# Performance work log

Measured on AMD Instinct MI355X. Metric: run time of the kernel, lower is better.

The kernel has to match this reference:

```python
import jax, jax.numpy as jnp
import numpy as np

NUM_CLASSES = 32
SIGMA = 0.02
LOG_SIGMA = float(np.log(SIGMA))
HALF_LOG_2PI = float(0.5 * np.log(2.0 * np.pi))


def _gcn(x, adj, W1, b1, W2, b2):
    # Two-layer GCN: h = relu(A x W1 + b1); out = A h W2 + b2
    h = jax.nn.relu(jnp.einsum('bij,bjf->bif', adj, x) @ W1 + b1)
    return jnp.einsum('bij,bjf->bif', adj, h) @ W2 + b2


def setup_inputs() -> dict:
    key = jax.random.key(0)
    ks = jax.random.split(key, 10)
    B, N, F = 64, 1024, 512
    x = jax.random.normal(ks[0], (B, N, F), dtype=jnp.float32)
    adj = jax.random.uniform(ks[1], (B, N, N), dtype=jnp.float32) / N  # row-scaled dense adjacency
    masks = jax.random.randint(ks[2], (B, N, F), 0, 2, dtype=jnp.int32)
    noise = jax.random.normal(ks[3], (B, N, F), dtype=jnp.float32)
    s = 0.05
    We1 = jax.random.normal(ks[4], (F, 30), dtype=jnp.float32) * s
    be1 = jnp.zeros((30,), dtype=jnp.float32)
    We2 = jax.random.normal(ks[5], (30, 18), dtype=jnp.float32) * s
    be2 = jnp.zeros((18,), dtype=jnp.float32)
    Wd1 = jax.random.normal(ks[6], (18, 30), dtype=jnp.float32) * s
    bd1 = jnp.zeros((30,), dtype=jnp.float32)
    Wd2 = jax.random.normal(ks[7], (30, F), dtype=jnp.float32) * s
    bd2 = jnp.zeros((F,), dtype=jnp.float32)
    return dict(x=x, adj=adj, masks=masks, noise=noise, We1=We1, be1=be1,
                We2=We2, be2=be2, Wd1=Wd1, bd1=bd1, Wd2=Wd2, bd2=bd2)


def reference(x, adj, masks, noise, We1, be1, We2, be2, Wd1, bd1, Wd2, bd2):
    enc = _gcn(x, adj, We1, be1, We2, be2)            # [B,N,18]
    dec = _gcn(enc, adj, Wd1, bd1, Wd2, bd2)          # [B,N,F]
    dec_act = jnp.concatenate(
        (jax.nn.softmax(dec[..., :NUM_CLASSES], axis=-1),
         jax.nn.sigmoid(dec[..., NUM_CLASSES:])), axis=-1)
    m = masks.astype(dec_act.dtype)
    # Vectorized masked reparameterized Gaussian sample: s = mu + sigma*eps
    sampled = dec_act + m * (SIGMA * noise)
    # log N(s; mu, sigma) = -eps^2/2 - log(sigma) - 0.5*log(2pi), summed over masked entries
    lp_elem = -0.5 * noise * noise - LOG_SIGMA - HALF_LOG_2PI
    log_probs = jnp.sum(m * lp_elem, axis=(1, 2))      # [B]
    return dec, sampled, log_probs
```

## Files before the change

### kernel.cpp

```cpp
#include <hip/hip_runtime.h>

#define B_ 64
#define NN 1024
#define FF 512

typedef float  fx4 __attribute__((ext_vector_type(4)));
typedef float  fx2 __attribute__((ext_vector_type(2)));
typedef int    ix4 __attribute__((ext_vector_type(4)));
typedef unsigned int   ux4i __attribute__((ext_vector_type(4)));
typedef unsigned int   ux2i __attribute__((ext_vector_type(2)));
typedef unsigned short us4  __attribute__((ext_vector_type(4)));
typedef short  sx8 __attribute__((ext_vector_type(8)));

#define FP8_SCALE   16384.0f
#define INV_SCALE   6.103515625e-5f

static __device__ __forceinline__ unsigned short f2bf(float f){
    union { float f; unsigned u; } v; v.f = f;
    unsigned r = v.u + 0x7FFFu + ((v.u >> 16) & 1u);
    return (unsigned short)(r >> 16);
}
static __device__ __forceinline__ float bf2f(unsigned short h){
    union { unsigned u; float f; } v; v.u = ((unsigned)h) << 16;
    return v.f;
}
static __device__ __forceinline__ unsigned cvt_pk_bf16(float lo, float hi){
    unsigned r;
    asm("v_cvt_pk_bf16_f32 %0, %1, %2" : "=v"(r) : "v"(lo), "v"(hi));
    return r;
}
static __device__ __forceinline__ sx8 pack_bf16x8(fx4 v0, fx4 v1){
    union { unsigned u[4]; sx8 s; } r;
    r.u[0] = cvt_pk_bf16(v0[0], v0[1]);
    r.u[1] = cvt_pk_bf16(v0[2], v0[3]);
    r.u[2] = cvt_pk_bf16(v1[0], v1[1]);
    r.u[3] = cvt_pk_bf16(v1[2], v1[3]);
    return r.s;
}
template<typename T>
static __device__ __forceinline__ T ntload(const T* p){ return __builtin_nontemporal_load(p); }
static __device__ __forceinline__ void ntstore4(float* p, fx4 v){
    __builtin_nontemporal_store(v, (fx4*)p);
}

__global__ __launch_bounds__(512) void k_xw1(
    const float* __restrict__ x, const float* __restrict__ We1,
    unsigned short* __restrict__ u1T){
    __shared__ unsigned short wls[32*512];
    int tid = threadIdx.x;
    for (int i = tid; i < 32*512; i += 512){
        int col = i >> 9, k = i & 511;
        float v = (col < 30) ? We1[k*30 + col] : 0.f;
        wls[col*512 + ((((k >> 3) ^ (col & 7)) << 3) | (k & 7))] = f2bf(v);
    }
    __syncthreads();
    int w = tid >> 6, l = tid & 63;
    int lr = l & 15, kq = l >> 4;
    int b = blockIdx.y;
    int rowb = blockIdx.x*128 + w*16;
    const float* xp = x + ((size_t)b*NN + rowb + lr)*FF + kq*8;
    fx4 acc0 = {0,0,0,0}, acc1 = {0,0,0,0};
    int c0 = lr, c1 = 16 + lr;
    #pragma unroll 4
    for (int kk = 0; kk < FF; kk += 32){
        fx4 v0 = ntload((const fx4*)(xp + kk));
        fx4 v1 = ntload((const fx4*)(xp + kk + 4));
        sx8 a = pack_bf16x8(v0, v1);
        int chunk = (kk >> 3) + kq;
        sx8 b0 = *(const sx8*)(wls + c0*512 + ((chunk ^ (c0 & 7)) << 3));
        sx8 b1 = *(const sx8*)(wls + c1*512 + ((chunk ^ (c1 & 7)) << 3));
        acc0 = __builtin_amdgcn_mfma_f32_16x16x32_bf16(a, b0, acc0, 0, 0, 0);
        acc1 = __builtin_amdgcn_mfma_f32_16x16x32_bf16(a, b1, acc1, 0, 0, 0);
    }
    int row0 = rowb + kq*4;
    us4 o0 = { f2bf(acc0[0]), f2bf(acc0[1]), f2bf(acc0[2]), f2bf(acc0[3]) };
    us4 o1 = { f2bf(acc1[0]), f2bf(acc1[1]), f2bf(acc1[2]), f2bf(acc1[3]) };
    *(us4*)(u1T + ((size_t)b*32 + c0)*NN + row0) = o0;
    *(us4*)(u1T + ((size_t)b*32 + c1)*NN + row0) = o1;
}

__global__ __launch_bounds__(256) void k_cvt_h1u2(
    const float* __restrict__ adjf, unsigned char* __restrict__ adj8,
    const unsigned short* __restrict__ uT, const float* __restrict__ be1,
    const float* __restrict__ We2, unsigned short* __restrict__ u2T){
    __shared__ unsigned short uts[32*NN];
    __shared__ unsigned short hls[128][34];
    __shared__ float wels[540];
    int tid = threadIdx.x;
    int rt = blockIdx.x, b = blockIdx.y;
    for (int i = tid; i < 540; i += 256) wels[i] = We2[i];
    const ux4i* src = (const ux4i*)(uT + (size_t)b*32*NN);
    #pragma unroll
    for (int i = 0; i < 16; i++){
        int j = tid + i*256;
        int c = j >> 7;
        ux4i v = src[j];
        *(ux4i*)((char*)uts + ((j*16) ^ ((c & 7) << 4))) = v;
    }
    __syncthreads();
    int w = tid >> 6, l = tid & 63;
    int lr = l & 15, lk = (l >> 4) * 8;
    size_t aoff = (size_t)b*NN*NN + (size_t)(rt*128 + w*32 + lr)*NN + lk;
    int c0 = lr, c1 = 16 + lr;
    fx4 acc00 = {0,0,0,0}, acc01 = {0,0,0,0}, acc10 = {0,0,0,0}, acc11 = {0,0,0,0};
    #pragma unroll 4
    for (int kk = 0; kk < NN; kk += 32){
        fx4 v00 = ntload((const fx4*)(adjf + aoff + kk));
        fx4 v01 = ntload((const fx4*)(adjf + aoff + kk + 4));
        fx4 v10 = ntload((const fx4*)(adjf + aoff + 16*NN + kk));
        fx4 v11 = ntload((const fx4*)(adjf + aoff + 16*NN + kk + 4));
        sx8 a0 = pack_bf16x8(v00, v01);
        sx8 a1 = pack_bf16x8(v10, v11);
        {
            const float S = FP8_SCALE;
            int d0 = __builtin_amdgcn_cvt_pk_fp8_f32(v00[0]*S, v00[1]*S, 0, false);
            d0     = __builtin_amdgcn_cvt_pk_fp8_f32(v00[2]*S, v00[3]*S, d0, true);
            int d1 = __builtin_amdgcn_cvt_pk_fp8_f32(v01[0]*S, v01[1]*S, 0, false);
            d1     = __builtin_amdgcn_cvt_pk_fp8_f32(v01[2]*S, v01[3]*S, d1, true);
            ux2i s0 = { (unsigned)d0, (unsigned)d1 };
            *(ux2i*)(adj8 + aoff + kk) = s0;
            int d2 = __builtin_amdgcn_cvt_pk_fp8_f32(v10[0]*S, v10[1]*S, 0, false);
            d2     = __builtin_amdgcn_cvt_pk_fp8_f32(v10[2]*S, v10[3]*S, d2, true);
            int d3 = __builtin_amdgcn_cvt_pk_fp8_f32(v11[0]*S, v11[1]*S, 0, false);
            d3     = __builtin_amdgcn_cvt_pk_fp8_f32(v11[2]*S, v11[3]*S, d3, true);
            ux2i s1 = { (unsigned)d2, (unsigned)d3 };
            *(ux2i*)(adj8 + aoff + 16*NN + kk) = s1;
        }
        int kb = (kk + lk) * 2;
        sx8 b0 = *(const sx8*)((const char*)uts + ((c0*2048 + kb) ^ ((c0 & 7) << 4)));
        sx8 b1 = *(const sx8*)((const char*)uts + ((c1*2048 + kb) ^ ((c1 & 7) << 4)));
        acc00 = __builtin_amdgcn_mfma_f32_16x16x32_bf16(a0, b0, acc00, 0, 0, 0);
        acc01 = __builtin_amdgcn_mfma_f32_16x16x32_bf16(a0, b1, acc01, 0, 0, 0);
        acc10 = __builtin_amdgcn_mfma_f32_16x16x32_bf16(a1, b0, acc10, 0, 0, 0);
        acc11 = __builtin_amdgcn_mfma_f32_16x16x32_bf16(a1, b1, acc11, 0, 0, 0);
    }
    float bias0 = (c0 < 30) ? be1[c0] : 0.f;
    float bias1 = (c1 < 30) ? be1[c1] : 0.f;
    int lq = l >> 4;
    #pragma unroll
    for (int mt = 0; mt < 2; mt++){
        int rl0 = w*32 + mt*16 + lq*4;
        fx4 am0 = mt ? acc10 : acc00;
        fx4 am1 = mt ? acc11 : acc01;
        #pragma unroll
        for (int ct = 0; ct < 2; ct++){
            fx4 a = ct ? am1 : am0;
            float bb = ct ? bias1 : bias0;
            int col = ct ? c1 : c0;
            #pragma unroll
            for (int j = 0; j < 4; j++)
                hls[rl0 + j][col] = f2bf(fmaxf(a[j] + bb, 0.f));
        }
    }
    __syncthreads();
    int row = tid >> 1, half = tid & 1;
    float h[30];
    #pragma unroll
    for (int j = 0; j < 30; j++) h[j] = bf2f(hls[row][j]);
    float acc2[9] = {0,0,0,0,0,0,0,0,0};
    #pragma unroll
    for (int j = 0; j < 30; j++){
        #pragma unroll
        for (int c = 0; c < 9; c++) acc2[c] += h[j]*wels[j*18 + half*9 + c];
    }
    unsigned short* base = u2T + (size_t)b*32*NN + rt*128 + row;
    #pragma unroll
    for (int c = 0; c < 9; c++)
        base[(size_t)(half*9 + c)*NN] = f2bf(acc2[c]*INV_SCALE);
    #pragma unroll
    for (int i = 0; i < 7; i++)
        base[(size_t)(18 + half*7 + i)*NN] = 0;
}

template<int RM>
__global__ __launch_bounds__(256) void k_adjf8(
    const unsigned char* __restrict__ adj8,
    const unsigned short* __restrict__ uT,
    const float* __restrict__ bias, int biasN, float oscale,
    unsigned short* __restrict__ outT){
    __shared__ unsigned short uts[32*NN];
    int tid = threadIdx.x;
    int rt = blockIdx.x, b = blockIdx.y;
    const ux4i* src = (const ux4i*)(uT + (size_t)b*32*NN);
    #pragma unroll
    for (int i = 0; i < 16; i++){
        int j = tid + i*256;
        int c = j >> 7;
        ux4i v = src[j];
        *(ux4i*)((char*)uts + ((j*16) ^ ((c & 7) << 4))) = v;
    }
    __syncthreads();
    int w = tid >> 6, l = tid & 63;
    int lr = l & 15, lk = (l >> 4) * 8;
    size_t aoff = (size_t)b*NN*NN + (size_t)(rt*128 + w*32 + lr)*NN + lk;
    int c0 = lr, c1 = 16 + lr;
    fx4 acc00 = {0,0,0,0}, acc01 = {0,0,0,0}, acc10 = {0,0,0,0}, acc11 = {0,0,0,0};
    #pragma unroll 4
    for (int kk = 0; kk < NN; kk += 32){
        ux2i q0 = *(const ux2i*)(adj8 + aoff + kk);
        ux2i q1 = *(const ux2i*)(adj8 + aoff + 16*NN + kk);
        fx2 f0 = __builtin_amdgcn_cvt_pk_f32_fp8((int)q0[0], false);
        fx2 f1 = __builtin_amdgcn_cvt_pk_f32_fp8((int)q0[0], true);
        fx2 f2 = __builtin_amdgcn_cvt_pk_f32_fp8((int)q0[1], false);
        fx2 f3 = __builtin_amdgcn_cvt_pk_f32_fp8((int)q0[1], true);
        fx2 g0 = __builtin_amdgcn_cvt_pk_f32_fp8((int)q1[0], false);
        fx2 g1 = __builtin_amdgcn_cvt_pk_f32_fp8((int)q1[0], true);
        fx2 g2 = __builtin_amdgcn_cvt_pk_f32_fp8((int)q1[1], false);
        fx2 g3 = __builtin_amdgcn_cvt_pk_f32_fp8((int)q1[1], true);
        union { unsigned u[4]; sx8 s; } A0, A1;
        A0.u[0] = cvt_pk_bf16(f0[0], f0[1]);
        A0.u[1] = cvt_pk_bf16(f1[0], f1[1]);
        A0.u[2] = cvt_pk_bf16(f2[0], f2[1]);
        A0.u[3] = cvt_pk_bf16(f3[0], f3[1]);
        A1.u[0] = cvt_pk_bf16(g0[0], g0[1]);
        A1.u[1] = cvt_pk_bf16(g1[0], g1[1]);
        A1.u[2] = cvt_pk_bf16(g2[0], g2[1]);
        A1.u[3] = cvt_pk_bf16(g3[0], g3[1]);
        int kb = (kk + lk) * 2;
        sx8 b0 = *(const sx8*)((const char*)uts + ((c0*2048 + kb) ^ ((c0 & 7) << 4)));
        sx8 b1 = *(const sx8*)((const char*)uts + ((c1*2048 + kb) ^ ((c1 & 7) << 4)));
        acc00 = __builtin_amdgcn_mfma_f32_16x16x32_bf16(A0.s, b0, acc00, 0, 0, 0);
        acc01 = __builtin_amdgcn_mfma_f32_16x16x32_bf16(A0.s, b1, acc01, 0, 0, 0);
        acc10 = __builtin_amdgcn_mfma_f32_16x16x32_bf16(A1.s, b0, acc10, 0, 0, 0);
        acc11 = __builtin_amdgcn_mfma_f32_16x16x32_bf16(A1.s, b1, acc11, 0, 0, 0);
    }
    float bias0 = 0.f, bias1 = 0.f;
    if (bias){
        if (c0 < biasN) bias0 = bias[c0];
        if (c1 < biasN) bias1 = bias[c1];
    }
    int lq = l >> 4;
    #pragma unroll
    for (int mt = 0; mt < 2; mt++){
        int row0 = rt*128 + w*32 + mt*16 + lq*4;
        fx4 am0 = mt ? acc10 : acc00;
        fx4 am1 = mt ? acc11 : acc01;
        #pragma unroll
        for (int ct = 0; ct < 2; ct++){
            fx4 a = ct ? am1 : am0;
            float bb = ct ? bias1 : bias0;
            int col = ct ? c1 : c0;
            us4 o;
            #pragma unroll
            for (int j = 0; j < 4; j++){
                float v = (a[j] + bb) * oscale;
                o[j] = f2bf(v);
            }
            if (RM){
                #pragma unroll
                for (int j = 0; j < 4; j++)
                    outT[((size_t)b*NN + row0 + j)*32 + col] = o[j];
            } else {
                *(us4*)(outT + ((size_t)b*32 + col)*NN + row0) = o;
            }
        }
    }
}

__global__ __launch_bounds__(256) void k_v1h2(
    const unsigned char* __restrict__ adj8,
    const unsigned short* __restrict__ encT,
    const float* __restrict__ Wd1, const float* __restrict__ bd1,
    unsigned short* __restrict__ h2T){
    __shared__ unsigned short uts[32*NN];
    __shared__ unsigned short vls[128][34];
    __shared__ float wd[540];
    __shared__ float bdl[30];
    int tid = threadIdx.x;
    int rt = blockIdx.x, b = blockIdx.y;
    for (int i = tid; i < 540; i += 256) wd[i] = Wd1[i];
    if (tid < 30) bdl[tid] = bd1[tid];
    const ux4i* src = (const ux4i*)(encT + (size_t)b*32*NN);
    #pragma unroll
    for (int i = 0; i < 16; i++){
        int j = tid + i*256;
        int c = j >> 7;
        ux4i v = src[j];
        *(ux4i*)((char*)uts + ((j*16) ^ ((c & 7) << 4))) = v;
    }
    __syncthreads();
    int w = tid >> 6, l = tid & 63;
    int lr = l & 15, lk = (l >> 4) * 8;
    size_t aoff = (size_t)b*NN*NN + (size_t)(rt*128 + w*32 + lr)*NN + lk;
    int c0 = lr, c1 = 16 + lr;
    fx4 acc00 = {0,0,0,0}, acc01 = {0,0,0,0}, acc10 = {0,0,0,0}, acc11 = {0,0,0,0};
    #pragma unroll 4
    for (int kk = 0; kk < NN; kk += 32){
        ux2i q0 = *(const ux2i*)(adj8 + aoff + kk);
        ux2i q1 = *(const ux2i*)(adj8 + aoff + 16*NN + kk);
        fx2 f0 = __builtin_amdgcn_cvt_pk_f32_fp8((int)q0[0], false);
        fx2 f1 = __builtin_amdgcn_cvt_pk_f32_fp8((int)q0[0], true);
        fx2 f2 = __builtin_amdgcn_cvt_pk_f32_fp8((int)q0[1], false);
        fx2 f3 = __builtin_amdgcn_cvt_pk_f32_fp8((int)q0[1], true);
        fx2 g0 = __builtin_amdgcn_cvt_pk_f32_fp8((int)q1[0], false);
        fx2 g1 = __builtin_amdgcn_cvt_pk_f32_fp8((int)q1[0], true);
        fx2 g2 = __builtin_amdgcn_cvt_pk_f32_fp8((int)q1[1], false);
        fx2 g3 = __builtin_amdgcn_cvt_pk_f32_fp8((int)q1[1], true);
        union { unsigned u[4]; sx8 s; } A0, A1;
        A0.u[0] = cvt_pk_bf16(f0[0], f0[1]);
        A0.u[1] = cvt_pk_bf16(f1[0], f1[1]);
        A0.u[2] = cvt_pk_bf16(f2[0], f2[1]);
        A0.u[3] = cvt_pk_bf16(f3[0], f3[1]);
        A1.u[0] = cvt_pk_bf16(g0[0], g0[1]);
        A1.u[1] = cvt_pk_bf16(g1[0], g1[1]);
        A1.u[2] = cvt_pk_bf16(g2[0], g2[1]);
        A1.u[3] = cvt_pk_bf16(g3[0], g3[1]);
        int kb = (kk + lk) * 2;
        sx8 b0 = *(const sx8*)((const char*)uts + ((c0*2048 + kb) ^ ((c0 & 7) << 4)));
        sx8 b1 = *(const sx8*)((const char*)uts + ((c1*2048 + kb) ^ ((c1 & 7) << 4)));
        acc00 = __builtin_amdgcn_mfma_f32_16x16x32_bf16(A0.s, b0, acc00, 0, 0, 0);
        acc01 = __builtin_amdgcn_mfma_f32_16x16x32_bf16(A0.s, b1, acc01, 0, 0, 0);
        acc10 = __builtin_amdgcn_mfma_f32_16x16x32_bf16(A1.s, b0, acc10, 0, 0, 0);
        acc11 = __builtin_amdgcn_mfma_f32_16x16x32_bf16(A1.s, b1, acc11, 0, 0, 0);
    }
    int lq = l >> 4;
    #pragma unroll
    for (int mt = 0; mt < 2; mt++){
        int rl0 = w*32 + mt*16 + lq*4;
        fx4 am0 = mt ? acc10 : acc00;
        fx4 am1 = mt ? acc11 : acc01;
        #pragma unroll
        for (int ct = 0; ct < 2; ct++){
            fx4 a = ct ? am1 : am0;
            int col = ct ? c1 : c0;
            #pragma unroll
            for (int j = 0; j < 4; j++)
                vls[rl0 + j][col] = f2bf(a[j]);
        }
    }
    __syncthreads();
    int row = tid >> 1, half = tid & 1;
    float v[18];
    #pragma unroll
    for (int j = 0; j < 18; j++) v[j] = bf2f(vls[row][j]);
    float acc2[15];
    #pragma unroll
    for (int c = 0; c < 15; c++) acc2[c] = 0.f;
    #pragma unroll
    for (int j = 0; j < 18; j++){
        #pragma unroll
        for (int c = 0; c < 15; c++) acc2[c] += v[j]*wd[j*30 + half*15 + c];
    }
    unsigned short* base = h2T + (size_t)b*32*NN + rt*128 + row;
    #pragma unroll
    for (int c = 0; c < 15; c++){
        int cc = half*15 + c;
        base[(size_t)cc*NN] = f2bf(fmaxf(acc2[c] + bdl[cc], 0.f)*INV_SCALE);
    }
    base[(size_t)(30 + half)*NN] = 0;
}

__global__ __launch_bounds__(1024) void k_v2dec(
    const unsigned char* __restrict__ adj8,
    const unsigned short* __restrict__ h2T,
    const float* __restrict__ Wd2, const float* __restrict__ bd2,
    const int* __restrict__ masks, const float* __restrict__ noise,
    float* __restrict__ dec, float* __restrict__ sampled, float* __restrict__ part){
    __shared__ __align__(16) char smem[127488];
    __shared__ float red[16];
    unsigned short* uts = (unsigned short*)smem;
    unsigned short* wls = (unsigned short*)smem;
    unsigned short* v2ls = (unsigned short*)(smem + 107008);
    int tid = threadIdx.x;
    int rt = blockIdx.x, b = blockIdx.y;
    int w = tid >> 6, l = tid & 63;
    int lr = l & 15, kq = l >> 4, lk = kq*8;
    const ux4i* src = (const ux4i*)(h2T + (size_t)b*32*NN);
    #pragma unroll
    for (int i = 0; i < 4; i++){
        int j = tid + i*1024;
        int c = j >> 7;
        ux4i v = src[j];
        *(ux4i*)((char*)uts + ((j*16) ^ ((c & 7) << 4))) = v;
    }
    __syncthreads();
    size_t aoff = (size_t)b*NN*NN + (size_t)(rt*256 + w*16 + lr)*NN + lk;
    int c0 = lr, c1 = 16 + lr;
    fx4 acc00 = {0,0,0,0}, acc01 = {0,0,0,0};
    #pragma unroll 4
    for (int kk = 0; kk < NN; kk += 32){
        ux2i q0 = *(const ux2i*)(adj8 + aoff + kk);
        fx2 f0 = __builtin_amdgcn_cvt_pk_f32_fp8((int)q0[0], false);
        fx2 f1 = __builtin_amdgcn_cvt_pk_f32_fp8((int)q0[0], true);
        fx2 f2 = __builtin_amdgcn_cvt_pk_f32_fp8((int)q0[1], false);
        fx2 f3 = __builtin_amdgcn_cvt_pk_f32_fp8((int)q0[1], true);
        union { unsigned u[4]; sx8 s; } A0;
        A0.u[0] = cvt_pk_bf16(f0[0], f0[1]);
        A0.u[1] = cvt_pk_bf16(f1[0], f1[1]);
        A0.u[2] = cvt_pk_bf16(f2[0], f2[1]);
        A0.u[3] = cvt_pk_bf16(f3[0], f3[1]);
        int kb = (kk + lk) * 2;
        sx8 b0 = *(const sx8*)((const char*)uts + ((c0*2048 + kb) ^ ((c0 & 7) << 4)));
        sx8 b1 = *(const sx8*)((const char*)uts + ((c1*2048 + kb) ^ ((c1 & 7) << 4)));
        acc00 = __builtin_amdgcn_mfma_f32_16x16x32_bf16(A0.s, b0, acc00, 0, 0, 0);
        acc01 = __builtin_amdgcn_mfma_f32_16x16x32_bf16(A0.s, b1, acc01, 0, 0, 0);
    }
    {
        int rl0 = w*16 + kq*4;
        #pragma unroll
        for (int ct = 0; ct < 2; ct++){
            fx4 a = ct ? acc01 : acc00;
            int col = ct ? c1 : c0;
            #pragma unroll
            for (int j = 0; j < 4; j++)
                v2ls[(rl0 + j)*40 + col] = f2bf(a[j]);
        }
    }
    __syncthreads();
    for (int i = tid; i < 512*32; i += 1024){
        int col = i & 511, k = i >> 9;
        float v = (k < 30) ? Wd2[k*512 + col] : 0.f;
        wls[col*40 + k] = f2bf(v);
    }
    __syncthreads();
    const float LPC = 2.9930844722234733f;
    float lpacc = 0.f;
    int growbase = b*NN + rt*256;
    for (int it = 0; it < 16; it++){
        int rb = it*16;
        float (*dls)[516] = (float(*)[516])(smem + 40960 + (it & 1)*33024);
        size_t offA = (size_t)(growbase + rb + w)*FF + l*8;
        ix4 mA0 = ntload((const ix4*)(masks + offA));
        ix4 mA1 = ntload((const ix4*)(masks + offA + 4));
        fx4 zA0 = ntload((const fx4*)(noise + offA));
        fx4 zA1 = ntload((const fx4*)(noise + offA + 4));
        sx8 a = *(const sx8*)(v2ls + (rb + lr)*40 + kq*8);
        #pragma unroll
        for (int i = 0; i < 2; i++){
            int c = (w + 16*i)*16 + lr;
            sx8 bb = *(const sx8*)(wls + c*40 + kq*8);
            fx4 acc = {0,0,0,0};
            acc = __builtin_amdgcn_mfma_f32_16x16x32_bf16(a, bb, acc, 0, 0, 0);
            float bi = bd2[c];
            #pragma unroll
            for (int j = 0; j < 4; j++)
                dls[kq*4 + j][c] = acc[j] + bi;
        }
        __syncthreads();
        {
            fx4 d0 = *(const fx4*)&dls[w][l*8];
            fx4 d1 = *(const fx4*)&dls[w][l*8 + 4];
            float av[8];
            #pragma unroll
            for (int i = 0; i < 4; i++){
                av[i]   = 1.f/(1.f + __expf(-d0[i]));
                av[4+i] = 1.f/(1.f + __expf(-d1[i]));
            }
            if (l < 4){
                float mx = d0[0];
                #pragma unroll
                for (int i = 1; i < 4; i++) mx = fmaxf(mx, d0[i]);
                #pragma unroll
                for (int i = 0; i < 4; i++) mx = fmaxf(mx, d1[i]);
                mx = fmaxf(mx, __shfl_xor(mx, 1, 4));
                mx = fmaxf(mx, __shfl_xor(mx, 2, 4));
                float e[8], ss = 0.f;
                #pragma unroll
                for (int i = 0; i < 4; i++){ e[i] = __expf(d0[i] - mx); ss += e[i]; }
                #pragma unroll
                for (int i = 0; i < 4; i++){ e[4+i] = __expf(d1[i] - mx); ss += e[4+i]; }
                ss += __shfl_xor(ss, 1, 4);
                ss += __shfl_xor(ss, 2, 4);
                float inv = 1.f / ss;
                #pragma unroll
                for (int i = 0; i < 8; i++) av[i] = e[i]*inv;
            }
            ntstore4(dec + offA,     d0);
            ntstore4(dec + offA + 4, d1);
            fx4 sm0, sm1;
            #pragma unroll
            for (int i = 0; i < 4; i++){
                float mi0 = (float)mA0[i], zi0 = zA0[i];
                float mi1 = (float)mA1[i], zi1 = zA1[i];
                sm0[i] = av[i]   + mi0*(0.02f*zi0);
                sm1[i] = av[4+i] + mi1*(0.02f*zi1);
                lpacc = fmaf(mi0, LPC - 0.5f*zi0*zi0, lpacc);
                lpacc = fmaf(mi1, LPC - 0.5f*zi1*zi1, lpacc);
            }
            ntstore4(sampled + offA,     sm0);
            ntstore4(sampled + offA + 4, sm1);
        }
    }
    #pragma unroll
    for (int off = 32; off > 0; off >>= 1) lpacc += __shfl_xor(lpacc, off);
    if (l == 0) red[w] = lpacc;
    __syncthreads();
    if (tid == 0){
        float s = 0.f;
        #pragma unroll
        for (int i = 0; i < 16; i++) s += red[i];
        part[blockIdx.y*4 + blockIdx.x] = s;
    }
}

__global__ __launch_bounds__(512, 2) void k_dec(
    const unsigned short* __restrict__ v2R,
    const float* __restrict__ Wd2, const float* __restrict__ bd2,
    const int* __restrict__ masks, const float* __restrict__ noise,
    float* __restrict__ dec, float* __restrict__ sampled, float* __restrict__ part){
    __shared__ unsigned short wls[512*40];
    __shared__ float dls[16][516];
    __shared__ float red[8];
    int tid = threadIdx.x;
    for (int i = tid; i < 512*32; i += 512){
        int col = i & 511, k = i >> 9;
        float v = (k < 30) ? Wd2[k*512 + col] : 0.f;
        wls[col*40 + k] = f2bf(v);
    }
    int w = tid >> 6, l = tid & 63;
    int lr = l & 15, kq = l >> 4;
    const float LPC = 2.9930844722234733f;
    float lpacc = 0.f;
    __syncthreads();
    #pragma unroll
    for (int it = 0; it < 4; it++){
        int rbase = blockIdx.x*64 + it*16;
        size_t offA = (size_t)(rbase + w)*FF + l*8;
        size_t offB = (size_t)(rbase + w + 8)*FF + l*8;
        ix4 mA0 = ntload((const ix4*)(masks + offA));
        ix4 mA1 = ntload((const ix4*)(masks + offA + 4));
        fx4 zA0 = ntload((const fx4*)(noise + offA));
        fx4 zA1 = ntload((const fx4*)(noise + offA + 4));
        ix4 mB0 = ntload((const ix4*)(masks + offB));
        ix4 mB1 = ntload((const ix4*)(masks + offB + 4));
        fx4 zB0 = ntload((const fx4*)(noise + offB));
        fx4 zB1 = ntload((const fx4*)(noise + offB + 4));
        sx8 a = *(const sx8*)(v2R + (size_t)(rbase + lr)*32 + kq*8);
        #pragma unroll
        for (int i = 0; i < 4; i++){
            int c = (w + 8*i)*16 + lr;
            sx8 bb = *(const sx8*)(wls + c*40 + kq*8);
            fx4 acc = {0,0,0,0};
            acc = __builtin_amdgcn_mfma_f32_16x16x32_bf16(a, bb, acc, 0, 0, 0);
            float bi = bd2[c];
            #pragma unroll
            for (int j = 0; j < 4; j++)
                dls[kq*4 + j][c] = acc[j] + bi;
        }
        __syncthreads();
        #pragma unroll
        for (int s = 0; s < 2; s++){
            int rloc = s ? (w + 8) : w;
            size_t off = s ? offB : offA;
            ix4 m0 = s ? mB0 : mA0;  ix4 m1 = s ? mB1 : mA1;
            fx4 z0 = s ? zB0 : zA0;  fx4 z1 = s ? zB1 : zA1;
            fx4 d0 = *(const fx4*)&dls[rloc][l*8];
            fx4 d1 = *(const fx4*)&dls[rloc][l*8 + 4];
            float av[8];
            #pragma unroll
            for (int i = 0; i < 4; i++){
                av[i]   = 1.f/(1.f + __expf(-d0[i]));
                av[4+i] = 1.f/(1.f + __expf(-d1[i]));
            }
            if (l < 4){
                float mx = d0[0];
                #pragma unroll
                for (int i = 1; i < 4; i++) mx = fmaxf(mx, d0[i]);
                #pragma unroll
                for (int i = 0; i < 4; i++) mx = fmaxf(mx, d1[i]);
                mx = fmaxf(mx, __shfl_xor(mx, 1, 4));
                mx = fmaxf(mx, __shfl_xor(mx, 2, 4));
                float e[8], ss = 0.f;
                #pragma unroll
                for (int i = 0; i < 4; i++){ e[i] = __expf(d0[i] - mx); ss += e[i]; }
                #pragma unroll
                for (int i = 0; i < 4; i++){ e[4+i] = __expf(d1[i] - mx); ss += e[4+i]; }
                ss += __shfl_xor(ss, 1, 4);
                ss += __shfl_xor(ss, 2, 4);
                float inv = 1.f / ss;
                #pragma unroll
                for (int i = 0; i < 8; i++) av[i] = e[i]*inv;
            }
            ntstore4(dec + off,     d0);
            ntstore4(dec + off + 4, d1);
            fx4 sm0, sm1;
            #pragma unroll
            for (int i = 0; i < 4; i++){
                float mi0 = (float)m0[i], zi0 = z0[i];
                float mi1 = (float)m1[i], zi1 = z1[i];
                sm0[i] = av[i]   + mi0*(0.02f*zi0);
                sm1[i] = av[4+i] + mi1*(0.02f*zi1);
                lpacc = fmaf(mi0, LPC - 0.5f*zi0*zi0, lpacc);
                lpacc = fmaf(mi1, LPC - 0.5f*zi1*zi1, lpacc);
            }
            ntstore4(sampled + off,     sm0);
            ntstore4(sampled + off + 4, sm1);
        }
        __syncthreads();
    }
    #pragma unroll
    for (int off = 32; off > 0; off >>= 1) lpacc += __shfl_xor(lpacc, off);
    if (l == 0) red[w] = lpacc;
    __syncthreads();
    if (tid == 0){
        float s = 0.f;
        #pragma unroll
        for (int i = 0; i < 8; i++) s += red[i];
        part[blockIdx.x] = s;
    }
}

template<int PB>
__global__ void k_lp(const float* __restrict__ part, float* __restrict__ logp){
    int t = threadIdx.x;
    float s = 0.f;
    #pragma unroll
    for (int i = 0; i < PB; i++) s += part[t*PB + i];
    logp[t] = s;
}

extern "C" void kernel_launch(void* const* d_in, const int* in_sizes, int n_in,
                              void* d_out, int out_size, void* d_ws, size_t ws_size,
                              hipStream_t stream){
    const float* x     = (const float*)d_in[0];
    const float* adj   = (const float*)d_in[1];
    const int*   masks = (const int*)  d_in[2];
    const float* noise = (const float*)d_in[3];
    const float* We1   = (const float*)d_in[4];
    const float* be1   = (const float*)d_in[5];
    const float* We2   = (const float*)d_in[6];
    const float* be2   = (const float*)d_in[7];
    const float* Wd1   = (const float*)d_in[8];
    const float* bd1   = (const float*)d_in[9];
    const float* Wd2   = (const float*)d_in[10];
    const float* bd2   = (const float*)d_in[11];

    float* dec     = (float*)d_out;
    float* sampled = dec + (size_t)B_*NN*FF;
    float* logp    = sampled + (size_t)B_*NN*FF;

    const size_t ADJ8_BYTES = (size_t)B_*NN*NN;
    const size_t BUF_ELEMS  = (size_t)B_*32*NN;
    bool bigws = ws_size >= ADJ8_BYTES + 4*BUF_ELEMS + 1024;

    unsigned char* adj8;
    unsigned short *bufA, *bufB;
    if (bigws){
        adj8 = (unsigned char*)d_ws;
        bufA = (unsigned short*)((char*)d_ws + ADJ8_BYTES);
        bufB = bufA + BUF_ELEMS;
    } else {
        adj8 = (unsigned char*)d_out;
        bufA = (unsigned short*)d_ws;
        bufB = bufA + BUF_ELEMS;
    }

    k_xw1<<<dim3(8, B_), 512, 0, stream>>>(x, We1, bufA);
    k_cvt_h1u2<<<dim3(8, B_), 256, 0, stream>>>(adj, adj8, bufA, be1, We2, bufB);
    k_adjf8<0><<<dim3(8, B_), 256, 0, stream>>>(adj8, bufB, be2, 18, INV_SCALE, bufA);
    k_v1h2<<<dim3(8, B_), 256, 0, stream>>>(adj8, bufA, Wd1, bd1, bufB);
    if (bigws){
        float* part = (float*)bufA;
        k_v2dec<<<dim3(4, B_), 1024, 0, stream>>>(adj8, bufB, Wd2, bd2, masks, noise,
                                                  dec, sampled, part);
        k_lp<4><<<1, 64, 0, stream>>>(part, logp);
    } else {
        float* part = (float*)bufB;
        k_adjf8<1><<<dim3(8, B_), 256, 0, stream>>>(adj8, bufB, nullptr, 0, 1.0f, bufA);
        k_dec<<<1024, 512, 0, stream>>>(bufA, Wd2, bd2, masks, noise, dec, sampled, part);
        k_lp<16><<<1, 64, 0, stream>>>(part, logp);
    }
}
```

Baseline: 324.3 us.

## Drop fused v2dec path; prefetch mask/noise in k_dec and use regular stores

Removes the fused k_v2dec kernel (adjacency GEMM plus decoder epilogue in 256 blocks of 1024 threads) and always runs the separate k_adjf8<1> pass followed by k_dec with 1024 blocks. In k_dec, the mask and noise loads for the next 16-row tile are issued before the current tile's epilogue, so they overlap with compute. Nontemporal stores for dec and sampled become ordinary stores. This trades one extra launch and an intermediate write/read of the aggregated features for much higher parallelism in the bandwidth-heavy epilogue, at the cost of more registers held by the prefetch.

```diff
diff --git a/kernel.cpp b/kernel.cpp
--- a/kernel.cpp
+++ b/kernel.cpp
@@ -39,9 +39,6 @@
 }
 template<typename T>
 static __device__ __forceinline__ T ntload(const T* p){ return __builtin_nontemporal_load(p); }
-static __device__ __forceinline__ void ntstore4(float* p, fx4 v){
-    __builtin_nontemporal_store(v, (fx4*)p);
-}
 
 __global__ __launch_bounds__(512) void k_xw1(
     const float* __restrict__ x, const float* __restrict__ We1,
@@ -350,149 +347,6 @@
     base[(size_t)(30 + half)*NN] = 0;
 }
 
-__global__ __launch_bounds__(1024) void k_v2dec(
-    const unsigned char* __restrict__ adj8,
-    const unsigned short* __restrict__ h2T,
-    const float* __restrict__ Wd2, const float* __restrict__ bd2,
-    const int* __restrict__ masks, const float* __restrict__ noise,
-    float* __restrict__ dec, float* __restrict__ sampled, float* __restrict__ part){
-    __shared__ __align__(16) char smem[127488];
-    __shared__ float red[16];
-    unsigned short* uts = (unsigned short*)smem;
-    unsigned short* wls = (unsigned short*)smem;
-    unsigned short* v2ls = (unsigned short*)(smem + 107008);
-    int tid = threadIdx.x;
-    int rt = blockIdx.x, b = blockIdx.y;
-    int w = tid >> 6, l = tid & 63;
-    int lr = l & 15, kq = l >> 4, lk = kq*8;
-    const ux4i* src = (const ux4i*)(h2T + (size_t)b*32*NN);
-    #pragma unroll
-    for (int i = 0; i < 4; i++){
-        int j = tid + i*1024;
-        int c = j >> 7;
-        ux4i v = src[j];
-        *(ux4i*)((char*)uts + ((j*16) ^ ((c & 7) << 4))) = v;
-    }
-    __syncthreads();
-    size_t aoff = (size_t)b*NN*NN + (size_t)(rt*256 + w*16 + lr)*NN + lk;
-    int c0 = lr, c1 = 16 + lr;
-    fx4 acc00 = {0,0,0,0}, acc01 = {0,0,0,0};
-    #pragma unroll 4
-    for (int kk = 0; kk < NN; kk += 32){
-        ux2i q0 = *(const ux2i*)(adj8 + aoff + kk);
-        fx2 f0 = __builtin_amdgcn_cvt_pk_f32_fp8((int)q0[0], false);
-        fx2 f1 = __builtin_amdgcn_cvt_pk_f32_fp8((int)q0[0], true);
-        fx2 f2 = __builtin_amdgcn_cvt_pk_f32_fp8((int)q0[1], false);
-        fx2 f3 = __builtin_amdgcn_cvt_pk_f32_fp8((int)q0[1], true);
-        union { unsigned u[4]; sx8 s; } A0;
-        A0.u[0] = cvt_pk_bf16(f0[0], f0[1]);
-        A0.u[1] = cvt_pk_bf16(f1[0], f1[1]);
-        A0.u[2] = cvt_pk_bf16(f2[0], f2[1]);
-        A0.u[3] = cvt_pk_bf16(f3[0], f3[1]);
-        int kb = (kk + lk) * 2;
-        sx8 b0 = *(const sx8*)((const char*)uts + ((c0*2048 + kb) ^ ((c0 & 7) << 4)));
-        sx8 b1 = *(const sx8*)((const char*)uts + ((c1*2048 + kb) ^ ((c1 & 7) << 4)));
-        acc00 = __builtin_amdgcn_mfma_f32_16x16x32_bf16(A0.s, b0, acc00, 0, 0, 0);
-        acc01 = __builtin_amdgcn_mfma_f32_16x16x32_bf16(A0.s, b1, acc01, 0, 0, 0);
-    }
-    {
-        int rl0 = w*16 + kq*4;
-        #pragma unroll
-        for (int ct = 0; ct < 2; ct++){
-            fx4 a = ct ? acc01 : acc00;
-            int col = ct ? c1 : c0;
-            #pragma unroll
-            for (int j = 0; j < 4; j++)
-                v2ls[(rl0 + j)*40 + col] = f2bf(a[j]);
-        }
-    }
-    __syncthreads();
-    for (int i = tid; i < 512*32; i += 1024){
-        int col = i & 511, k = i >> 9;
-        float v = (k < 30) ? Wd2[k*512 + col] : 0.f;
-        wls[col*40 + k] = f2bf(v);
-    }
-    __syncthreads();
-    const float LPC = 2.9930844722234733f;
-    float lpacc = 0.f;
-    int growbase = b*NN + rt*256;
-    for (int it = 0; it < 16; it++){
-        int rb = it*16;
-        float (*dls)[516] = (float(*)[516])(smem + 40960 + (it & 1)*33024);
-        size_t offA = (size_t)(growbase + rb + w)*FF + l*8;
-        ix4 mA0 = ntload((const ix4*)(masks + offA));
-        ix4 mA1 = ntload((const ix4*)(masks + offA + 4));
-        fx4 zA0 = ntload((const fx4*)(noise + offA));
-        fx4 zA1 = ntload((const fx4*)(noise + offA + 4));
-        sx8 a = *(const sx8*)(v2ls + (rb + lr)*40 + kq*8);
-        #pragma unroll
-        for (int i = 0; i < 2; i++){
-            int c = (w + 16*i)*16 + lr;
-            sx8 bb = *(const sx8*)(wls + c*40 + kq*8);
-            fx4 acc = {0,0,0,0};
-            acc = __builtin_amdgcn_mfma_f32_16x16x32_bf16(a, bb, acc, 0, 0, 0);
-            float bi = bd2[c];
-            #pragma unroll
-            for (int j = 0; j < 4; j++)
-                dls[kq*4 + j][c] = acc[j] + bi;
-        }
-        __syncthreads();
-        {
-            fx4 d0 = *(const fx4*)&dls[w][l*8];
-            fx4 d1 = *(const fx4*)&dls[w][l*8 + 4];
-            float av[8];
-            #pragma unroll
-            for (int i = 0; i < 4; i++){
-                av[i]   = 1.f/(1.f + __expf(-d0[i]));
-                av[4+i] = 1.f/(1.f + __expf(-d1[i]));
-            }
-            if (l < 4){
-                float mx = d0[0];
-                #pragma unroll
-                for (int i = 1; i < 4; i++) mx = fmaxf(mx, d0[i]);
-                #pragma unroll
-                for (int i = 0; i < 4; i++) mx = fmaxf(mx, d1[i]);
-                mx = fmaxf(mx, __shfl_xor(mx, 1, 4));
-                mx = fmaxf(mx, __shfl_xor(mx, 2, 4));
-                float e[8], ss = 0.f;
-                #pragma unroll
-                for (int i = 0; i < 4; i++){ e[i] = __expf(d0[i] - mx); ss += e[i]; }
-                #pragma unroll
-                for (int i = 0; i < 4; i++){ e[4+i] = __expf(d1[i] - mx); ss += e[4+i]; }
-                ss += __shfl_xor(ss, 1, 4);
-                ss += __shfl_xor(ss, 2, 4);
-                float inv = 1.f / ss;
-                #pragma unroll
-                for (int i = 0; i < 8; i++) av[i] = e[i]*inv;
-            }
-            ntstore4(dec + offA,     d0);
-            ntstore4(dec + offA + 4, d1);
-            fx4 sm0, sm1;
-            #pragma unroll
-            for (int i = 0; i < 4; i++){
-                float mi0 = (float)mA0[i], zi0 = zA0[i];
-                float mi1 = (float)mA1[i], zi1 = zA1[i];
-                sm0[i] = av[i]   + mi0*(0.02f*zi0);
-                sm1[i] = av[4+i] + mi1*(0.02f*zi1);
-                lpacc = fmaf(mi0, LPC - 0.5f*zi0*zi0, lpacc);
-                lpacc = fmaf(mi1, LPC - 0.5f*zi1*zi1, lpacc);
-            }
-            ntstore4(sampled + offA,     sm0);
-            ntstore4(sampled + offA + 4, sm1);
-        }
-    }
-    #pragma unroll
-    for (int off = 32; off > 0; off >>= 1) lpacc += __shfl_xor(lpacc, off);
-    if (l == 0) red[w] = lpacc;
-    __syncthreads();
-    if (tid == 0){
-        float s = 0.f;
-        #pragma unroll
-        for (int i = 0; i < 16; i++) s += red[i];
-        part[blockIdx.y*4 + blockIdx.x] = s;
-    }
-}
-
 __global__ __launch_bounds__(512, 2) void k_dec(
     const unsigned short* __restrict__ v2R,
     const float* __restrict__ Wd2, const float* __restrict__ bd2,
@@ -511,20 +365,20 @@
     int lr = l & 15, kq = l >> 4;
     const float LPC = 2.9930844722234733f;
     float lpacc = 0.f;
+    size_t offA = (size_t)(blockIdx.x*64 + w)*FF + l*8;
+    size_t offB = offA + (size_t)8*FF;
+    ix4 mA0 = ntload((const ix4*)(masks + offA));
+    ix4 mA1 = ntload((const ix4*)(masks + offA + 4));
+    fx4 zA0 = ntload((const fx4*)(noise + offA));
+    fx4 zA1 = ntload((const fx4*)(noise + offA + 4));
+    ix4 mB0 = ntload((const ix4*)(masks + offB));
+    ix4 mB1 = ntload((const ix4*)(masks + offB + 4));
+    fx4 zB0 = ntload((const fx4*)(noise + offB));
+    fx4 zB1 = ntload((const fx4*)(noise + offB + 4));
     __syncthreads();
     #pragma unroll
     for (int it = 0; it < 4; it++){
         int rbase = blockIdx.x*64 + it*16;
-        size_t offA = (size_t)(rbase + w)*FF + l*8;
-        size_t offB = (size_t)(rbase + w + 8)*FF + l*8;
-        ix4 mA0 = ntload((const ix4*)(masks + offA));
-        ix4 mA1 = ntload((const ix4*)(masks + offA + 4));
-        fx4 zA0 = ntload((const fx4*)(noise + offA));
-        fx4 zA1 = ntload((const fx4*)(noise + offA + 4));
-        ix4 mB0 = ntload((const ix4*)(masks + offB));
-        ix4 mB1 = ntload((const ix4*)(masks + offB + 4));
-        fx4 zB0 = ntload((const fx4*)(noise + offB));
-        fx4 zB1 = ntload((const fx4*)(noise + offB + 4));
         sx8 a = *(const sx8*)(v2R + (size_t)(rbase + lr)*32 + kq*8);
         #pragma unroll
         for (int i = 0; i < 4; i++){
@@ -538,6 +392,20 @@
                 dls[kq*4 + j][c] = acc[j] + bi;
         }
         __syncthreads();
+        ix4 nmA0, nmA1, nmB0, nmB1; fx4 nzA0, nzA1, nzB0, nzB1;
+        size_t noffA = 0, noffB = 0;
+        if (it < 3){
+            noffA = (size_t)(rbase + 16 + w)*FF + l*8;
+            noffB = noffA + (size_t)8*FF;
+            nmA0 = ntload((const ix4*)(masks + noffA));
+            nmA1 = ntload((const ix4*)(masks + noffA + 4));
+            nzA0 = ntload((const fx4*)(noise + noffA));
+            nzA1 = ntload((const fx4*)(noise + noffA + 4));
+            nmB0 = ntload((const ix4*)(masks + noffB));
+            nmB1 = ntload((const ix4*)(masks + noffB + 4));
+            nzB0 = ntload((const fx4*)(noise + noffB));
+            nzB1 = ntload((const fx4*)(noise + noffB + 4));
+        }
         #pragma unroll
         for (int s = 0; s < 2; s++){
             int rloc = s ? (w + 8) : w;
@@ -571,8 +439,8 @@
                 #pragma unroll
                 for (int i = 0; i < 8; i++) av[i] = e[i]*inv;
             }
-            ntstore4(dec + off,     d0);
-            ntstore4(dec + off + 4, d1);
+            *(fx4*)(dec + off)     = d0;
+            *(fx4*)(dec + off + 4) = d1;
             fx4 sm0, sm1;
             #pragma unroll
             for (int i = 0; i < 4; i++){
@@ -583,10 +451,15 @@
                 lpacc = fmaf(mi0, LPC - 0.5f*zi0*zi0, lpacc);
                 lpacc = fmaf(mi1, LPC - 0.5f*zi1*zi1, lpacc);
             }
-            ntstore4(sampled + off,     sm0);
-            ntstore4(sampled + off + 4, sm1);
+            *(fx4*)(sampled + off)     = sm0;
+            *(fx4*)(sampled + off + 4) = sm1;
         }
         __syncthreads();
+        if (it < 3){
+            offA = noffA; offB = noffB;
+            mA0 = nmA0; mA1 = nmA1; zA0 = nzA0; zA1 = nzA1;
+            mB0 = nmB0; mB1 = nmB1; zB0 = nzB0; zB1 = nzB1;
+        }
     }
     #pragma unroll
     for (int off = 32; off > 0; off >>= 1) lpacc += __shfl_xor(lpacc, off);
@@ -631,7 +504,7 @@
 
     const size_t ADJ8_BYTES = (size_t)B_*NN*NN;
     const size_t BUF_ELEMS  = (size_t)B_*32*NN;
-    bool bigws = ws_size >= ADJ8_BYTES + 4*BUF_ELEMS + 1024;
+    bool bigws = ws_size >= ADJ8_BYTES + 4*BUF_ELEMS + 4096;
 
     unsigned char* adj8;
     unsigned short *bufA, *bufB;
@@ -649,15 +522,8 @@
     k_cvt_h1u2<<<dim3(8, B_), 256, 0, stream>>>(adj, adj8, bufA, be1, We2, bufB);
     k_adjf8<0><<<dim3(8, B_), 256, 0, stream>>>(adj8, bufB, be2, 18, INV_SCALE, bufA);
     k_v1h2<<<dim3(8, B_), 256, 0, stream>>>(adj8, bufA, Wd1, bd1, bufB);
-    if (bigws){
-        float* part = (float*)bufA;
-        k_v2dec<<<dim3(4, B_), 1024, 0, stream>>>(adj8, bufB, Wd2, bd2, masks, noise,
-                                                  dec, sampled, part);
-        k_lp<4><<<1, 64, 0, stream>>>(part, logp);
-    } else {
-        float* part = (float*)bufB;
-        k_adjf8<1><<<dim3(8, B_), 256, 0, stream>>>(adj8, bufB, nullptr, 0, 1.0f, bufA);
-        k_dec<<<1024, 512, 0, stream>>>(bufA, Wd2, bd2, masks, noise, dec, sampled, part);
-        k_lp<16><<<1, 64, 0, stream>>>(part, logp);
-    }
-}
+    k_adjf8<1><<<dim3(8, B_), 256, 0, stream>>>(adj8, bufB, nullptr, 0, 1.0f, bufA);
+    float* part = (float*)bufB;
+    k_dec<<<1024, 512, 0, stream>>>(bufA, Wd2, bd2, masks, noise, dec, sampled, part);
+    k_lp<16><<<1, 64, 0, stream>>>(part, logp);
+}
```

Result: slower. 338.3 us (+4.3%).
